# Kernel optimization log

Measured on AMD Instinct MI355X. Metric: run time of the kernel, lower is better.

The kernel has to match this reference:

```python
import jax, jax.numpy as jnp
import numpy as np

V = 50257   # n_unique_words
C = 50257   # n_classes
E = 256     # embed_dim
H = 512     # h_dim
S_IN = 512
S_OUT = 511
START = 1


def setup_inputs() -> dict:
    key = jax.random.key(0)
    ks = jax.random.split(key, 12)
    s = 1.0 / np.sqrt(H)
    u = lambda k, shp: jax.random.uniform(k, shp, jnp.float32, -s, s)
    return {
        "h0": jnp.zeros((1, H), jnp.float32),
        "input_ids": jax.random.randint(ks[0], (1, S_IN), 0, V),
        "output_ids": jax.random.randint(ks[1], (1, S_OUT), 0, V),
        "emb": jax.random.normal(ks[2], (V, E), jnp.float32) * 0.02,
        "enc_wih": u(ks[3], (H, E)),
        "enc_whh": u(ks[4], (H, H)),
        "enc_bih": u(ks[5], (H,)),
        "enc_bhh": u(ks[5], (H,)),
        "dec_wih": u(ks[6], (H, E)),
        "dec_whh": u(ks[7], (H, H)),
        "dec_bih": u(ks[8], (H,)),
        "dec_bhh": u(ks[8], (H,)),
        "fc_w": u(ks[9], (C, H)),
        "fc_b": u(ks[10], (C,)),
    }


def _rnn_cell(x, h, wih, whh, bih, bhh):
    # Elman RNNCell: h' = tanh(x W_ih^T + b_ih + h W_hh^T + b_hh)
    return jnp.tanh(x @ wih.T + bih + h @ whh.T + bhh)


def reference(h0, input_ids, output_ids, emb, enc_wih, enc_whh, enc_bih, enc_bhh,
              dec_wih, dec_whh, dec_bih, dec_bhh, fc_w, fc_b):
    # ---- encode ----
    enc_xs = jnp.swapaxes(emb[input_ids], 0, 1)  # [S_in, 1, E]
    def enc_step(h, x):
        h = _rnn_cell(x, h, enc_wih, enc_whh, enc_bih, enc_bhh)
        return h, None
    hn, _ = jax.lax.scan(enc_step, h0, enc_xs)
    # ---- decode_train ----
    start_emb = emb[jnp.array([START])]          # [1, E]
    h1 = _rnn_cell(start_emb, hn, dec_wih, dec_whh, dec_bih, dec_bhh)
    dec_xs = jnp.swapaxes(emb[output_ids], 0, 1)  # [S_out, 1, E]
    def dec_step(h, x):
        h = _rnn_cell(x, h, dec_wih, dec_whh, dec_bih, dec_bhh)
        return h, h
    _, hs = jax.lax.scan(dec_step, h1, dec_xs)    # [S_out, 1, H]
    pred = jnp.concatenate([h1[None], hs], axis=0)[:, 0, :]  # [S_out+1, H]
    return pred @ fc_w.T + fc_b                   # [S_out+1, C]
```

## Files before the change

kernel.cpp:

```cpp
#include <hip/hip_runtime.h>
#include <hip/hip_fp16.h>

#define EDIM 256
#define HDIM 512
#define CDIM 50257
#define NT_FC 197
#define NJOBS (NT_FC * 4)

using half2_t = __attribute__((ext_vector_type(2))) _Float16;
using half8_t = __attribute__((ext_vector_type(8))) _Float16;
using float4_t = __attribute__((ext_vector_type(4))) float;

__device__ __forceinline__ float dot2(uint32_t w, uint32_t h, float acc) {
    return __builtin_amdgcn_fdot2(__builtin_bit_cast(half2_t, w),
                                  __builtin_bit_cast(half2_t, h), acc, false);
}

__device__ __forceinline__ float fast_tanh(float x) {
    float e = __builtin_amdgcn_exp2f(x * 2.8853900817779268f);
    return 1.f - 2.f * __builtin_amdgcn_rcpf(e + 1.f);
}

__device__ __forceinline__ void scan_body(
    const _Float16* __restrict__ wpack, const float* __restrict__ z,
    const _Float16* __restrict__ h_init, _Float16* __restrict__ hs_out,
    _Float16* __restrict__ hfin_out, int* prog, int nsteps,
    uint4* wlds, uint4* hbuf4) {
    const int tid = threadIdx.x;
    const int c = tid & 15;
    const int g_own = tid >> 3;
    const int hstore = 128 * (g_own & 3) + 8 * (g_own >> 2) + (tid & 7);

    const uint4* wp4 = (const uint4*)wpack;
    uint32_t wreg[192];
#pragma unroll
    for (int g = 0; g < 48; ++g) {
        uint4 v = wp4[g * 512 + tid];
        wreg[g * 4 + 0] = v.x; wreg[g * 4 + 1] = v.y;
        wreg[g * 4 + 2] = v.z; wreg[g * 4 + 3] = v.w;
    }
#pragma unroll
    for (int g = 48; g < 64; ++g) wlds[(g - 48) * 512 + tid] = wp4[g * 512 + tid];

    ((_Float16*)hbuf4)[hstore] = h_init ? h_init[tid] : (_Float16)0.f;
    __syncthreads();

    _Float16 hlast = (_Float16)0.f;
    int cur = 0;
    for (int t = 0; t < nsteps; ++t) {
        float zv = z[t * HDIM + tid];
        const uint4* hb = hbuf4 + cur * 64;
        float acc[16];
#pragma unroll
        for (int r = 0; r < 16; ++r) acc[r] = 0.f;
#pragma unroll
        for (int i = 0; i < 4; ++i) {
            uint4 hg = hb[i * 16 + c];
#pragma unroll
            for (int jr = 0; jr < 12; ++jr) {
                acc[jr] = dot2(wreg[(jr * 4 + i) * 4 + 0], hg.x, acc[jr]);
                acc[jr] = dot2(wreg[(jr * 4 + i) * 4 + 1], hg.y, acc[jr]);
                acc[jr] = dot2(wreg[(jr * 4 + i) * 4 + 2], hg.z, acc[jr]);
                acc[jr] = dot2(wreg[(jr * 4 + i) * 4 + 3], hg.w, acc[jr]);
            }
#pragma unroll
            for (int js = 0; js < 4; ++js) {
                uint4 w = wlds[(js * 4 + i) * 512 + tid];
                acc[12 + js] = dot2(w.x, hg.x, acc[12 + js]);
                acc[12 + js] = dot2(w.y, hg.y, acc[12 + js]);
                acc[12 + js] = dot2(w.z, hg.z, acc[12 + js]);
                acc[12 + js] = dot2(w.w, hg.w, acc[12 + js]);
            }
        }
        float s, keep;
#define FOLD_DPP(aL, aH, bit, ctrl, dst)                                      \
        s = (c & bit) ? (aL) : (aH);                                          \
        s = __builtin_bit_cast(float, __builtin_amdgcn_mov_dpp(               \
                __builtin_bit_cast(int, s), ctrl, 0xF, 0xF, true));           \
        keep = (c & bit) ? (aH) : (aL);                                       \
        dst = keep + s;
#define FOLD_SWZ(aL, aH, bit, pat, dst)                                       \
        s = (c & bit) ? (aL) : (aH);                                          \
        s = __builtin_bit_cast(float, __builtin_amdgcn_ds_swizzle(            \
                __builtin_bit_cast(int, s), pat));                            \
        keep = (c & bit) ? (aH) : (aL);                                       \
        dst = keep + s;
        float b0, b1, b2, b3, b4, b5, b6, b7, d0, d1, d2, d3, e0, e1, v;
        FOLD_DPP(acc[0],  acc[1],  1, 0xB1, b0)
        FOLD_DPP(acc[2],  acc[3],  1, 0xB1, b1)
        FOLD_DPP(acc[4],  acc[5],  1, 0xB1, b2)
        FOLD_DPP(acc[6],  acc[7],  1, 0xB1, b3)
        FOLD_DPP(acc[8],  acc[9],  1, 0xB1, b4)
        FOLD_DPP(acc[10], acc[11], 1, 0xB1, b5)
        FOLD_DPP(acc[12], acc[13], 1, 0xB1, b6)
        FOLD_DPP(acc[14], acc[15], 1, 0xB1, b7)
        FOLD_DPP(b0, b1, 2, 0x4E, d0)
        FOLD_DPP(b2, b3, 2, 0x4E, d1)
        FOLD_DPP(b4, b5, 2, 0x4E, d2)
        FOLD_DPP(b6, b7, 2, 0x4E, d3)
        FOLD_DPP(d0, d2, 8, 0x128, e0)
        FOLD_DPP(d1, d3, 8, 0x128, e1)
        FOLD_SWZ(e0, e1, 4, 0x101F, v)
#undef FOLD_DPP
#undef FOLD_SWZ
        float hnew = fast_tanh(v + zv);
        _Float16 h16v = (_Float16)hnew;
        ((_Float16*)hbuf4)[(cur ^ 1) * 512 + hstore] = h16v;
        if (hs_out) hs_out[t * HDIM + tid] = h16v;
        hlast = h16v;
        __syncthreads();
        if (prog && (t & 127) == 127 && tid == 0) {
            __threadfence();
            __hip_atomic_store(prog, t + 1, __ATOMIC_RELEASE,
                               __HIP_MEMORY_SCOPE_AGENT);
        }
        cur ^= 1;
    }
    if (hfin_out) hfin_out[tid] = hlast;
}

__global__ void __launch_bounds__(256) prep_a(
    const float* __restrict__ enc_whh, _Float16* __restrict__ wpe,
    const int* __restrict__ in_ids, const float* __restrict__ emb,
    const float* __restrict__ enc_wih, const float* __restrict__ enc_bih,
    const float* __restrict__ enc_bhh, float* __restrict__ z,
    int* __restrict__ prog) {
    __shared__ float x[EDIM];
    int b = blockIdx.x;
    if (b == 0 && threadIdx.x == 0)
        __hip_atomic_store(prog, 0, __ATOMIC_RELAXED, __HIP_MEMORY_SCOPE_AGENT);
    if (b < 128) {
        int idx = b * 256 + threadIdx.x;
        int g = idx >> 9, t = idx & 511;
        int jr = g >> 2, i = g & 3;
        int row = ((t >> 4) << 4) + jr;
        int k0 = ((t & 15) << 5) + (i << 3);
        const float* src = enc_whh + row * HDIM + k0;
        uint32_t d[4];
#pragma unroll
        for (int q = 0; q < 4; ++q) {
            half2_t p;
            p[0] = (_Float16)src[2 * q];
            p[1] = (_Float16)src[2 * q + 1];
            d[q] = __builtin_bit_cast(uint32_t, p);
        }
        ((uint4*)wpe)[g * 512 + t] = make_uint4(d[0], d[1], d[2], d[3]);
    } else {
        int t = b - 128;
        int id = in_ids[t];
        x[threadIdx.x] = emb[(long)id * EDIM + threadIdx.x];
        __syncthreads();
#pragma unroll
        for (int rr = 0; rr < 2; ++rr) {
            int r = threadIdx.x + rr * 256;
            const float4* w4 = (const float4*)(enc_wih + r * EDIM);
            float acc = 0.f;
#pragma unroll 8
            for (int k4 = 0; k4 < 64; ++k4) {
                float4 wv = w4[k4];
                acc += wv.x * x[k4 * 4 + 0] + wv.y * x[k4 * 4 + 1] +
                       wv.z * x[k4 * 4 + 2] + wv.w * x[k4 * 4 + 3];
            }
            z[t * HDIM + r] = acc + enc_bih[r] + enc_bhh[r];
        }
    }
}

__global__ void __launch_bounds__(512, 2) enc_fused(
    const _Float16* __restrict__ wpe, const float* __restrict__ z,
    _Float16* __restrict__ hn16,
    const float* __restrict__ dec_whh, _Float16* __restrict__ wpd,
    const int* __restrict__ out_ids, const float* __restrict__ emb,
    const float* __restrict__ dec_wih, const float* __restrict__ dec_bih,
    const float* __restrict__ dec_bhh, float* __restrict__ zf,
    const float* __restrict__ fc_w, _Float16* __restrict__ fcw16, long fcw_n) {
    __shared__ uint4 wlds[16 * 512];
    __shared__ uint4 hbuf4[2 * 64];
    int b = blockIdx.x, tid = threadIdx.x;
    if (b == 0) {
        scan_body(wpe, z, nullptr, nullptr, hn16, nullptr, 512, wlds, hbuf4);
    } else if (b < 65) {
        int idx = (b - 1) * 512 + tid;
        int g = idx >> 9, t = idx & 511;
        int jr = g >> 2, i = g & 3;
        int row = ((t >> 4) << 4) + jr;
        int k0 = ((t & 15) << 5) + (i << 3);
        const float* src = dec_whh + row * HDIM + k0;
        uint32_t d[4];
#pragma unroll
        for (int q = 0; q < 4; ++q) {
            half2_t p;
            p[0] = (_Float16)src[2 * q];
            p[1] = (_Float16)src[2 * q + 1];
            d[q] = __builtin_bit_cast(uint32_t, p);
        }
        ((uint4*)wpd)[g * 512 + t] = make_uint4(d[0], d[1], d[2], d[3]);
    } else if (b < 577) {
        int t = 512 + (b - 65);
        float* x = (float*)wlds;
        int id = (t == 512) ? 1 : out_ids[t - 513];
        if (tid < EDIM) x[tid] = emb[(long)id * EDIM + tid];
        __syncthreads();
        const float4* w4 = (const float4*)(dec_wih + tid * EDIM);
        float acc = 0.f;
#pragma unroll 8
        for (int k4 = 0; k4 < 64; ++k4) {
            float4 wv = w4[k4];
            acc += wv.x * x[k4 * 4 + 0] + wv.y * x[k4 * 4 + 1] +
                   wv.z * x[k4 * 4 + 2] + wv.w * x[k4 * 4 + 3];
        }
        zf[t * HDIM + tid] = acc + dec_bih[tid] + dec_bhh[tid];
    } else {
        long i = ((long)(b - 577) * 512 + tid) * 8;
        if (i + 8 <= fcw_n) {
            const float4* s4 = (const float4*)(fc_w + i);
            float4 a = s4[0], bb = s4[1];
            half8_t o;
            o[0] = (_Float16)a.x;  o[1] = (_Float16)a.y;
            o[2] = (_Float16)a.z;  o[3] = (_Float16)a.w;
            o[4] = (_Float16)bb.x; o[5] = (_Float16)bb.y;
            o[6] = (_Float16)bb.z; o[7] = (_Float16)bb.w;
            *(half8_t*)(fcw16 + i) = o;
        }
    }
}

__global__ void __launch_bounds__(512, 2) dec_fc(
    const _Float16* __restrict__ wpd, const float* __restrict__ zdec,
    const _Float16* __restrict__ hn16, _Float16* __restrict__ h16,
    int* __restrict__ prog,
    const _Float16* __restrict__ Bw16, const float* __restrict__ Bw32,
    int use16, const float* __restrict__ bias, float* __restrict__ out) {
    __shared__ uint4 wlds[16 * 512];
    __shared__ uint4 hbuf4[2 * 64];
    int b = blockIdx.x, tid = threadIdx.x;
    if (b == 0) {
        scan_body(wpd, zdec, hn16, h16, nullptr, prog, 512, wlds, hbuf4);
        return;
    }
    int w = tid >> 6, l = tid & 63;
    int wm = (w >> 2) * 64, wn = (w & 3) * 64;
    int lr = l & 15, lk = (l >> 4) * 8;
    for (int j = b - 1; j < NJOBS; j += 255) {
        int mj = j / NT_FC, nj = j - mj * NT_FC;
        if (tid == 0) {
            int need = (mj + 1) * 128;
            while (__hip_atomic_load(prog, __ATOMIC_RELAXED,
                                     __HIP_MEMORY_SCOPE_AGENT) < need)
                __builtin_amdgcn_s_sleep(64);
            __threadfence();
        }
        __syncthreads();
        int m0 = mj * 128, n0 = nj * 256;
        float4_t acc[4][4];
#pragma unroll
        for (int fm = 0; fm < 4; ++fm)
#pragma unroll
            for (int fn = 0; fn < 4; ++fn)
                acc[fm][fn] = (float4_t){0.f, 0.f, 0.f, 0.f};
        for (int ks = 0; ks < 512; ks += 32) {
            half8_t a[4], bf[4];
#pragma unroll
            for (int f = 0; f < 4; ++f) {
                int m = m0 + wm + f * 16 + lr;
                a[f] = *(const half8_t*)(h16 + (long)m * 512 + ks + lk);
                int n = n0 + wn + f * 16 + lr;
                if (n < CDIM) {
                    if (use16) {
                        bf[f] = *(const half8_t*)(Bw16 + (long)n * 512 + ks + lk);
                    } else {
                        const float4* bp4 =
                            (const float4*)(Bw32 + (long)n * 512 + ks + lk);
                        float4 x0 = bp4[0], x1 = bp4[1];
                        half8_t bb;
                        bb[0] = (_Float16)x0.x; bb[1] = (_Float16)x0.y;
                        bb[2] = (_Float16)x0.z; bb[3] = (_Float16)x0.w;
                        bb[4] = (_Float16)x1.x; bb[5] = (_Float16)x1.y;
                        bb[6] = (_Float16)x1.z; bb[7] = (_Float16)x1.w;
                        bf[f] = bb;
                    }
                } else {
#pragma unroll
                    for (int e = 0; e < 8; ++e) bf[f][e] = (_Float16)0.f;
                }
            }
#pragma unroll
            for (int fm = 0; fm < 4; ++fm)
#pragma unroll
                for (int fn = 0; fn < 4; ++fn)
                    acc[fm][fn] = __builtin_amdgcn_mfma_f32_16x16x32_f16(
                        a[fm], bf[fn], acc[fm][fn], 0, 0, 0);
        }
#pragma unroll
        for (int fn = 0; fn < 4; ++fn) {
            int n = n0 + wn + fn * 16 + lr;
            if (n >= CDIM) continue;
            float bv = bias[n];
#pragma unroll
            for (int fm = 0; fm < 4; ++fm) {
#pragma unroll
                for (int q = 0; q < 4; ++q) {
                    int m = m0 + wm + fm * 16 + (l >> 4) * 4 + q;
                    out[(long)m * CDIM + n] = acc[fm][fn][q] + bv;
                }
            }
        }
    }
}

extern "C" void kernel_launch(void* const* d_in, const int* in_sizes, int n_in,
                              void* d_out, int out_size, void* d_ws, size_t ws_size,
                              hipStream_t stream) {
    const int* input_ids  = (const int*)d_in[1];
    const int* output_ids = (const int*)d_in[2];
    const float* emb      = (const float*)d_in[3];
    const float* enc_wih  = (const float*)d_in[4];
    const float* enc_whh  = (const float*)d_in[5];
    const float* enc_bih  = (const float*)d_in[6];
    const float* enc_bhh  = (const float*)d_in[7];
    const float* dec_wih  = (const float*)d_in[8];
    const float* dec_whh  = (const float*)d_in[9];
    const float* dec_bih  = (const float*)d_in[10];
    const float* dec_bhh  = (const float*)d_in[11];
    const float* fc_w     = (const float*)d_in[12];
    const float* fc_b     = (const float*)d_in[13];
    float* out = (float*)d_out;

    char* ws = (char*)d_ws;
    float* z        = (float*)ws;
    _Float16* wpe   = (_Float16*)(ws + (2u << 20));
    _Float16* wpd   = (_Float16*)(ws + (2u << 20) + (512u << 10));
    _Float16* h16   = (_Float16*)(ws + (3u << 20));
    _Float16* hn16  = (_Float16*)(ws + (3u << 20) + (512u << 10));
    int* prog       = (int*)(ws + (3u << 20) + (513u << 10));
    _Float16* fcw16 = (_Float16*)(ws + (4u << 20));

    const long fcw_n = (long)CDIM * HDIM;
    bool use_f16_fc = ws_size >= (size_t)(4u << 20) + (size_t)fcw_n * 2;
    int nb_cvt = use_f16_fc ? (int)((fcw_n / 8 + 511) / 512) : 0;

    prep_a<<<640, 256, 0, stream>>>(enc_whh, wpe, input_ids, emb,
                                    enc_wih, enc_bih, enc_bhh, z, prog);
    enc_fused<<<577 + nb_cvt, 512, 0, stream>>>(
        wpe, z, hn16, dec_whh, wpd, output_ids, emb,
        dec_wih, dec_bih, dec_bhh, z, fc_w, fcw16, fcw_n);
    dec_fc<<<256, 512, 0, stream>>>(wpd, z + 512 * HDIM, hn16, h16, prog,
                                    fcw16, fc_w, use_f16_fc ? 1 : 0,
                                    fc_b, out);
}
```

Before: 1.492 ms.

## Split each RNN scan across two workgroups with global flag handshakes

Both the encoder and decoder recurrences now run on two workgroups, each owning half of the hidden rows and keeping its half of W_hh fully in registers. The hidden state is exchanged through global memory double buffers, and per-step release/acquire flags synchronise the pair. This halves the per-step dot-product work and removes the LDS-resident weight slice, but adds a cross-CU spin-wait and global round trip on every one of the 1024 sequential steps. The FC consumers now wait on both decoder flags, and block indices are remapped, presumably so the two scan blocks land on different XCDs or CUs.

```diff
diff --git a/kernel.cpp b/kernel.cpp
--- a/kernel.cpp
+++ b/kernel.cpp
@@ -21,57 +21,48 @@
     return 1.f - 2.f * __builtin_amdgcn_rcpf(e + 1.f);
 }
 
-__device__ __forceinline__ void scan_body(
-    const _Float16* __restrict__ wpack, const float* __restrict__ z,
-    const _Float16* __restrict__ h_init, _Float16* __restrict__ hs_out,
-    _Float16* __restrict__ hfin_out, int* prog, int nsteps,
-    uint4* wlds, uint4* hbuf4) {
+__device__ __forceinline__ void scan2_body(
+    const uint4* __restrict__ wp4,
+    const float* __restrict__ z,
+    _Float16* __restrict__ hxA, _Float16* __restrict__ hxB,
+    int* myflag, int* pflag,
+    _Float16* __restrict__ hs_out,
+    _Float16* __restrict__ hfin_out,
+    int hb2, int nsteps) {
     const int tid = threadIdx.x;
-    const int c = tid & 15;
-    const int g_own = tid >> 3;
-    const int hstore = 128 * (g_own & 3) + 8 * (g_own >> 2) + (tid & 7);
-
-    const uint4* wp4 = (const uint4*)wpack;
-    uint32_t wreg[192];
-#pragma unroll
-    for (int g = 0; g < 48; ++g) {
-        uint4 v = wp4[g * 512 + tid];
-        wreg[g * 4 + 0] = v.x; wreg[g * 4 + 1] = v.y;
-        wreg[g * 4 + 2] = v.z; wreg[g * 4 + 3] = v.w;
-    }
-#pragma unroll
-    for (int g = 48; g < 64; ++g) wlds[(g - 48) * 512 + tid] = wp4[g * 512 + tid];
-
-    ((_Float16*)hbuf4)[hstore] = h_init ? h_init[tid] : (_Float16)0.f;
-    __syncthreads();
-
-    _Float16 hlast = (_Float16)0.f;
-    int cur = 0;
+    const int c = tid & 15, rg = tid >> 4;
+    const int grow = hb2 * 256 + rg * 8 + (c & 7);
+
+    uint4 wreg4[32];
+#pragma unroll
+    for (int g = 0; g < 32; ++g) wreg4[g] = wp4[g * 512 + tid];
+
     for (int t = 0; t < nsteps; ++t) {
-        float zv = z[t * HDIM + tid];
-        const uint4* hb = hbuf4 + cur * 64;
-        float acc[16];
-#pragma unroll
-        for (int r = 0; r < 16; ++r) acc[r] = 0.f;
-#pragma unroll
-        for (int i = 0; i < 4; ++i) {
-            uint4 hg = hb[i * 16 + c];
-#pragma unroll
-            for (int jr = 0; jr < 12; ++jr) {
-                acc[jr] = dot2(wreg[(jr * 4 + i) * 4 + 0], hg.x, acc[jr]);
-                acc[jr] = dot2(wreg[(jr * 4 + i) * 4 + 1], hg.y, acc[jr]);
-                acc[jr] = dot2(wreg[(jr * 4 + i) * 4 + 2], hg.z, acc[jr]);
-                acc[jr] = dot2(wreg[(jr * 4 + i) * 4 + 3], hg.w, acc[jr]);
-            }
-#pragma unroll
-            for (int js = 0; js < 4; ++js) {
-                uint4 w = wlds[(js * 4 + i) * 512 + tid];
-                acc[12 + js] = dot2(w.x, hg.x, acc[12 + js]);
-                acc[12 + js] = dot2(w.y, hg.y, acc[12 + js]);
-                acc[12 + js] = dot2(w.z, hg.z, acc[12 + js]);
-                acc[12 + js] = dot2(w.w, hg.w, acc[12 + js]);
-            }
-        }
+        if (tid == 0) {
+            while (__hip_atomic_load(pflag, __ATOMIC_RELAXED,
+                                     __HIP_MEMORY_SCOPE_AGENT) < t) {}
+            __threadfence();
+        }
+        __syncthreads();
+        const _Float16* hcur = (t & 1) ? hxB : hxA;
+        _Float16*       hnxt = (t & 1) ? hxA : hxB;
+        float zv = z[t * HDIM + grow];
+        uint4 hg0 = ((const uint4*)hcur)[c * 4 + 0];
+        uint4 hg1 = ((const uint4*)hcur)[c * 4 + 1];
+        uint4 hg2 = ((const uint4*)hcur)[c * 4 + 2];
+        uint4 hg3 = ((const uint4*)hcur)[c * 4 + 3];
+
+        float acc[8] = {0.f, 0.f, 0.f, 0.f, 0.f, 0.f, 0.f, 0.f};
+#define MAC_I(I, HG)                                                          \
+        _Pragma("unroll")                                                     \
+        for (int jr = 0; jr < 8; ++jr) {                                      \
+            acc[jr] = dot2(wreg4[jr * 4 + I].x, HG.x, acc[jr]);               \
+            acc[jr] = dot2(wreg4[jr * 4 + I].y, HG.y, acc[jr]);               \
+            acc[jr] = dot2(wreg4[jr * 4 + I].z, HG.z, acc[jr]);               \
+            acc[jr] = dot2(wreg4[jr * 4 + I].w, HG.w, acc[jr]);               \
+        }
+        MAC_I(0, hg0) MAC_I(1, hg1) MAC_I(2, hg2) MAC_I(3, hg3)
+#undef MAC_I
         float s, keep;
 #define FOLD_DPP(aL, aH, bit, ctrl, dst)                                      \
         s = (c & bit) ? (aL) : (aH);                                          \
@@ -79,125 +70,113 @@
                 __builtin_bit_cast(int, s), ctrl, 0xF, 0xF, true));           \
         keep = (c & bit) ? (aH) : (aL);                                       \
         dst = keep + s;
-#define FOLD_SWZ(aL, aH, bit, pat, dst)                                       \
-        s = (c & bit) ? (aL) : (aH);                                          \
-        s = __builtin_bit_cast(float, __builtin_amdgcn_ds_swizzle(            \
-                __builtin_bit_cast(int, s), pat));                            \
-        keep = (c & bit) ? (aH) : (aL);                                       \
-        dst = keep + s;
-        float b0, b1, b2, b3, b4, b5, b6, b7, d0, d1, d2, d3, e0, e1, v;
-        FOLD_DPP(acc[0],  acc[1],  1, 0xB1, b0)
-        FOLD_DPP(acc[2],  acc[3],  1, 0xB1, b1)
-        FOLD_DPP(acc[4],  acc[5],  1, 0xB1, b2)
-        FOLD_DPP(acc[6],  acc[7],  1, 0xB1, b3)
-        FOLD_DPP(acc[8],  acc[9],  1, 0xB1, b4)
-        FOLD_DPP(acc[10], acc[11], 1, 0xB1, b5)
-        FOLD_DPP(acc[12], acc[13], 1, 0xB1, b6)
-        FOLD_DPP(acc[14], acc[15], 1, 0xB1, b7)
-        FOLD_DPP(b0, b1, 2, 0x4E, d0)
-        FOLD_DPP(b2, b3, 2, 0x4E, d1)
-        FOLD_DPP(b4, b5, 2, 0x4E, d2)
-        FOLD_DPP(b6, b7, 2, 0x4E, d3)
-        FOLD_DPP(d0, d2, 8, 0x128, e0)
-        FOLD_DPP(d1, d3, 8, 0x128, e1)
-        FOLD_SWZ(e0, e1, 4, 0x101F, v)
+        float f0, f1, f2, f3, g0, g1, e, v;
+        FOLD_DPP(acc[0], acc[1], 1, 0xB1, f0)
+        FOLD_DPP(acc[2], acc[3], 1, 0xB1, f1)
+        FOLD_DPP(acc[4], acc[5], 1, 0xB1, f2)
+        FOLD_DPP(acc[6], acc[7], 1, 0xB1, f3)
+        FOLD_DPP(f0, f1, 2, 0x4E, g0)
+        FOLD_DPP(f2, f3, 2, 0x4E, g1)
+        s = (c & 4) ? g0 : g1;
+        s = __builtin_bit_cast(float, __builtin_amdgcn_ds_swizzle(
+                __builtin_bit_cast(int, s), 0x101F));
+        keep = (c & 4) ? g1 : g0;
+        e = keep + s;
+        s = __builtin_bit_cast(float, __builtin_amdgcn_mov_dpp(
+                __builtin_bit_cast(int, e), 0x128, 0xF, 0xF, true));
+        v = e + s;
 #undef FOLD_DPP
-#undef FOLD_SWZ
         float hnew = fast_tanh(v + zv);
         _Float16 h16v = (_Float16)hnew;
-        ((_Float16*)hbuf4)[(cur ^ 1) * 512 + hstore] = h16v;
-        if (hs_out) hs_out[t * HDIM + tid] = h16v;
-        hlast = h16v;
+        if (c < 8) {
+            hnxt[grow] = h16v;
+            if (hs_out) hs_out[t * HDIM + grow] = h16v;
+            if (hfin_out && t == nsteps - 1) hfin_out[grow] = h16v;
+        }
         __syncthreads();
-        if (prog && (t & 127) == 127 && tid == 0) {
-            __threadfence();
-            __hip_atomic_store(prog, t + 1, __ATOMIC_RELEASE,
+        if (tid == 0)
+            __hip_atomic_store(myflag, t + 1, __ATOMIC_RELEASE,
                                __HIP_MEMORY_SCOPE_AGENT);
-        }
-        cur ^= 1;
-    }
-    if (hfin_out) hfin_out[tid] = hlast;
-}
-
-__global__ void __launch_bounds__(256) prep_a(
+    }
+}
+
+__device__ __forceinline__ void pack_one(const float* __restrict__ whh,
+                                         _Float16* __restrict__ wp, int G) {
+    int hb2 = G >> 14, g = (G >> 9) & 31, tt = G & 511;
+    int row = hb2 * 256 + ((tt >> 4) << 3) + (g >> 2);
+    int k0 = ((tt & 15) << 5) + ((g & 3) << 3);
+    const float* src = whh + row * HDIM + k0;
+    uint32_t d[4];
+#pragma unroll
+    for (int q = 0; q < 4; ++q) {
+        half2_t p;
+        p[0] = (_Float16)src[2 * q];
+        p[1] = (_Float16)src[2 * q + 1];
+        d[q] = __builtin_bit_cast(uint32_t, p);
+    }
+    ((uint4*)wp)[G] = make_uint4(d[0], d[1], d[2], d[3]);
+}
+
+__global__ void __launch_bounds__(512) prep_a(
     const float* __restrict__ enc_whh, _Float16* __restrict__ wpe,
     const int* __restrict__ in_ids, const float* __restrict__ emb,
     const float* __restrict__ enc_wih, const float* __restrict__ enc_bih,
     const float* __restrict__ enc_bhh, float* __restrict__ z,
-    int* __restrict__ prog) {
+    int* __restrict__ flags, _Float16* __restrict__ hx_enc) {
     __shared__ float x[EDIM];
-    int b = blockIdx.x;
-    if (b == 0 && threadIdx.x == 0)
-        __hip_atomic_store(prog, 0, __ATOMIC_RELAXED, __HIP_MEMORY_SCOPE_AGENT);
-    if (b < 128) {
-        int idx = b * 256 + threadIdx.x;
-        int g = idx >> 9, t = idx & 511;
-        int jr = g >> 2, i = g & 3;
-        int row = ((t >> 4) << 4) + jr;
-        int k0 = ((t & 15) << 5) + (i << 3);
-        const float* src = enc_whh + row * HDIM + k0;
-        uint32_t d[4];
-#pragma unroll
-        for (int q = 0; q < 4; ++q) {
-            half2_t p;
-            p[0] = (_Float16)src[2 * q];
-            p[1] = (_Float16)src[2 * q + 1];
-            d[q] = __builtin_bit_cast(uint32_t, p);
-        }
-        ((uint4*)wpe)[g * 512 + t] = make_uint4(d[0], d[1], d[2], d[3]);
-    } else {
-        int t = b - 128;
-        int id = in_ids[t];
-        x[threadIdx.x] = emb[(long)id * EDIM + threadIdx.x];
-        __syncthreads();
-#pragma unroll
-        for (int rr = 0; rr < 2; ++rr) {
-            int r = threadIdx.x + rr * 256;
-            const float4* w4 = (const float4*)(enc_wih + r * EDIM);
-            float acc = 0.f;
+    int b = blockIdx.x, tid = threadIdx.x;
+    if (b == 0) {
+        if (tid < 128)
+            __hip_atomic_store(flags + tid, 0, __ATOMIC_RELAXED,
+                               __HIP_MEMORY_SCOPE_AGENT);
+        hx_enc[tid] = (_Float16)0.f;
+        return;
+    }
+    if (b < 65) {
+        pack_one(enc_whh, wpe, (b - 1) * 512 + tid);
+        return;
+    }
+    int t = b - 65;
+    int id = in_ids[t];
+    if (tid < EDIM) x[tid] = emb[(long)id * EDIM + tid];
+    __syncthreads();
+    const float4* w4 = (const float4*)(enc_wih + tid * EDIM);
+    float acc = 0.f;
 #pragma unroll 8
-            for (int k4 = 0; k4 < 64; ++k4) {
-                float4 wv = w4[k4];
-                acc += wv.x * x[k4 * 4 + 0] + wv.y * x[k4 * 4 + 1] +
-                       wv.z * x[k4 * 4 + 2] + wv.w * x[k4 * 4 + 3];
-            }
-            z[t * HDIM + r] = acc + enc_bih[r] + enc_bhh[r];
-        }
-    }
+    for (int k4 = 0; k4 < 64; ++k4) {
+        float4 wv = w4[k4];
+        acc += wv.x * x[k4 * 4 + 0] + wv.y * x[k4 * 4 + 1] +
+               wv.z * x[k4 * 4 + 2] + wv.w * x[k4 * 4 + 3];
+    }
+    z[t * HDIM + tid] = acc + enc_bih[tid] + enc_bhh[tid];
 }
 
 __global__ void __launch_bounds__(512, 2) enc_fused(
     const _Float16* __restrict__ wpe, const float* __restrict__ z,
-    _Float16* __restrict__ hn16,
+    int* __restrict__ flags,
+    _Float16* __restrict__ hx_enc, _Float16* __restrict__ hx_dec,
     const float* __restrict__ dec_whh, _Float16* __restrict__ wpd,
     const int* __restrict__ out_ids, const float* __restrict__ emb,
     const float* __restrict__ dec_wih, const float* __restrict__ dec_bih,
     const float* __restrict__ dec_bhh, float* __restrict__ zf,
     const float* __restrict__ fc_w, _Float16* __restrict__ fcw16, long fcw_n) {
-    __shared__ uint4 wlds[16 * 512];
-    __shared__ uint4 hbuf4[2 * 64];
+    __shared__ uint4 ldsbig[16 * 512];
     int b = blockIdx.x, tid = threadIdx.x;
-    if (b == 0) {
-        scan_body(wpe, z, nullptr, nullptr, hn16, nullptr, 512, wlds, hbuf4);
-    } else if (b < 65) {
-        int idx = (b - 1) * 512 + tid;
-        int g = idx >> 9, t = idx & 511;
-        int jr = g >> 2, i = g & 3;
-        int row = ((t >> 4) << 4) + jr;
-        int k0 = ((t & 15) << 5) + (i << 3);
-        const float* src = dec_whh + row * HDIM + k0;
-        uint32_t d[4];
-#pragma unroll
-        for (int q = 0; q < 4; ++q) {
-            half2_t p;
-            p[0] = (_Float16)src[2 * q];
-            p[1] = (_Float16)src[2 * q + 1];
-            d[q] = __builtin_bit_cast(uint32_t, p);
-        }
-        ((uint4*)wpd)[g * 512 + t] = make_uint4(d[0], d[1], d[2], d[3]);
-    } else if (b < 577) {
-        int t = 512 + (b - 65);
-        float* x = (float*)wlds;
+    if (tid == 511) *(volatile unsigned int*)&ldsbig[0] = 0u;
+    if (b == 0 || b == 8) {
+        int hb2 = (b == 8) ? 1 : 0;
+        scan2_body((const uint4*)wpe + hb2 * 32 * 512, z,
+                   hx_enc, hx_enc + 512,
+                   flags + hb2 * 32, flags + (1 - hb2) * 32,
+                   nullptr, hx_dec, hb2, 512);
+        return;
+    }
+    int jb = (b < 8) ? b - 1 : b - 2;
+    if (jb < 64) {
+        pack_one(dec_whh, wpd, jb * 512 + tid);
+    } else if (jb < 576) {
+        int t = 512 + (jb - 64);
+        float* x = (float*)ldsbig;
         int id = (t == 512) ? 1 : out_ids[t - 513];
         if (tid < EDIM) x[tid] = emb[(long)id * EDIM + tid];
         __syncthreads();
@@ -211,7 +190,7 @@
         }
         zf[t * HDIM + tid] = acc + dec_bih[tid] + dec_bhh[tid];
     } else {
-        long i = ((long)(b - 577) * 512 + tid) * 8;
+        long i = ((long)(jb - 576) * 512 + tid) * 8;
         if (i + 8 <= fcw_n) {
             const float4* s4 = (const float4*)(fc_w + i);
             float4 a = s4[0], bb = s4[1];
@@ -227,25 +206,35 @@
 
 __global__ void __launch_bounds__(512, 2) dec_fc(
     const _Float16* __restrict__ wpd, const float* __restrict__ zdec,
-    const _Float16* __restrict__ hn16, _Float16* __restrict__ h16,
-    int* __restrict__ prog,
+    _Float16* __restrict__ hx_dec, _Float16* __restrict__ h16,
+    int* __restrict__ flags,
     const _Float16* __restrict__ Bw16, const float* __restrict__ Bw32,
     int use16, const float* __restrict__ bias, float* __restrict__ out) {
-    __shared__ uint4 wlds[16 * 512];
-    __shared__ uint4 hbuf4[2 * 64];
+    __shared__ uint4 ldsbig[16 * 512];
     int b = blockIdx.x, tid = threadIdx.x;
-    if (b == 0) {
-        scan_body(wpd, zdec, hn16, h16, nullptr, prog, 512, wlds, hbuf4);
+    if (tid == 511) *(volatile unsigned int*)&ldsbig[0] = 0u;
+    int* decf0 = flags + 64;
+    int* decf1 = flags + 96;
+    if (b == 0 || b == 8) {
+        int hb2 = (b == 8) ? 1 : 0;
+        scan2_body((const uint4*)wpd + hb2 * 32 * 512, zdec,
+                   hx_dec, hx_dec + 512,
+                   (hb2 ? decf1 : decf0), (hb2 ? decf0 : decf1),
+                   h16, nullptr, hb2, 512);
         return;
     }
+    if ((b & 7) == 0) return;
+    int di = b - (b >> 3) - 1;
     int w = tid >> 6, l = tid & 63;
     int wm = (w >> 2) * 64, wn = (w & 3) * 64;
     int lr = l & 15, lk = (l >> 4) * 8;
-    for (int j = b - 1; j < NJOBS; j += 255) {
+    for (int j = di; j < NJOBS; j += 224) {
         int mj = j / NT_FC, nj = j - mj * NT_FC;
         if (tid == 0) {
             int need = (mj + 1) * 128;
-            while (__hip_atomic_load(prog, __ATOMIC_RELAXED,
+            while (__hip_atomic_load(decf0, __ATOMIC_RELAXED,
+                                     __HIP_MEMORY_SCOPE_AGENT) < need ||
+                   __hip_atomic_load(decf1, __ATOMIC_RELAXED,
                                      __HIP_MEMORY_SCOPE_AGENT) < need)
                 __builtin_amdgcn_s_sleep(64);
             __threadfence();
@@ -331,20 +320,23 @@
     _Float16* wpe   = (_Float16*)(ws + (2u << 20));
     _Float16* wpd   = (_Float16*)(ws + (2u << 20) + (512u << 10));
     _Float16* h16   = (_Float16*)(ws + (3u << 20));
-    _Float16* hn16  = (_Float16*)(ws + (3u << 20) + (512u << 10));
-    int* prog       = (int*)(ws + (3u << 20) + (513u << 10));
+    int* flags      = (int*)(ws + (3u << 20) + (512u << 10));
+    _Float16* hx_enc = (_Float16*)(ws + (3u << 20) + (512u << 10) + 512);
+    _Float16* hx_dec = (_Float16*)(ws + (3u << 20) + (512u << 10) + 2560);
     _Float16* fcw16 = (_Float16*)(ws + (4u << 20));
 
     const long fcw_n = (long)CDIM * HDIM;
     bool use_f16_fc = ws_size >= (size_t)(4u << 20) + (size_t)fcw_n * 2;
     int nb_cvt = use_f16_fc ? (int)((fcw_n / 8 + 511) / 512) : 0;
 
-    prep_a<<<640, 256, 0, stream>>>(enc_whh, wpe, input_ids, emb,
-                                    enc_wih, enc_bih, enc_bhh, z, prog);
-    enc_fused<<<577 + nb_cvt, 512, 0, stream>>>(
-        wpe, z, hn16, dec_whh, wpd, output_ids, emb,
+    prep_a<<<577, 512, 0, stream>>>(enc_whh, wpe, input_ids, emb,
+                                    enc_wih, enc_bih, enc_bhh, z,
+                                    flags, hx_enc);
+    enc_fused<<<578 + nb_cvt, 512, 0, stream>>>(
+        wpe, z, flags, hx_enc, hx_dec,
+        dec_whh, wpd, output_ids, emb,
         dec_wih, dec_bih, dec_bhh, z, fc_w, fcw16, fcw_n);
-    dec_fc<<<256, 512, 0, stream>>>(wpd, z + 512 * HDIM, hn16, h16, prog,
+    dec_fc<<<256, 512, 0, stream>>>(wpd, z + 512 * HDIM, hx_dec, h16, flags,
                                     fcw16, fc_w, use_f16_fc ? 1 : 0,
                                     fc_b, out);
 }
```

Measured after the change: 2.124 ms (median of 2 runs). +42.4%, slower.

## Swizzle packed RNN weights to simplify reduction and idle every eighth FC block

Applied to the files above, without the earlier changes.

The recurrent weight packing now XORs the row index with the lane-in-group, so each lane's partial sums already line up for a simple DPP add tree. This drops the select/keep pairs around every reduction step on the serial scan's critical path. The FC consumer blocks also change: every eighth block exits immediately (after a dummy LDS write), leaving 224 worker blocks. The likely aim is to free the XCD or CU that hosts the scan block from contention, at the cost of less FC throughput.

```diff
diff --git a/kernel.cpp b/kernel.cpp
--- a/kernel.cpp
+++ b/kernel.cpp
@@ -19,6 +19,23 @@
 __device__ __forceinline__ float fast_tanh(float x) {
     float e = __builtin_amdgcn_exp2f(x * 2.8853900817779268f);
     return 1.f - 2.f * __builtin_amdgcn_rcpf(e + 1.f);
+}
+
+__device__ __forceinline__ void pack_one(const float* __restrict__ whh,
+                                         _Float16* __restrict__ wp,
+                                         int g, int t) {
+    int row = ((t >> 4) << 4) + ((g >> 2) ^ (t & 15));
+    int k0 = ((t & 15) << 5) + ((g & 3) << 3);
+    const float* src = whh + row * HDIM + k0;
+    uint32_t d[4];
+#pragma unroll
+    for (int q = 0; q < 4; ++q) {
+        half2_t p;
+        p[0] = (_Float16)src[2 * q];
+        p[1] = (_Float16)src[2 * q + 1];
+        d[q] = __builtin_bit_cast(uint32_t, p);
+    }
+    ((uint4*)wp)[g * 512 + t] = make_uint4(d[0], d[1], d[2], d[3]);
 }
 
 __device__ __forceinline__ void scan_body(
@@ -50,60 +67,55 @@
     for (int t = 0; t < nsteps; ++t) {
         float zv = z[t * HDIM + tid];
         const uint4* hb = hbuf4 + cur * 64;
-        float acc[16];
-#pragma unroll
-        for (int r = 0; r < 16; ++r) acc[r] = 0.f;
+        float f[16];
+#pragma unroll
+        for (int r = 0; r < 16; ++r) f[r] = 0.f;
 #pragma unroll
         for (int i = 0; i < 4; ++i) {
             uint4 hg = hb[i * 16 + c];
 #pragma unroll
-            for (int jr = 0; jr < 12; ++jr) {
-                acc[jr] = dot2(wreg[(jr * 4 + i) * 4 + 0], hg.x, acc[jr]);
-                acc[jr] = dot2(wreg[(jr * 4 + i) * 4 + 1], hg.y, acc[jr]);
-                acc[jr] = dot2(wreg[(jr * 4 + i) * 4 + 2], hg.z, acc[jr]);
-                acc[jr] = dot2(wreg[(jr * 4 + i) * 4 + 3], hg.w, acc[jr]);
+            for (int s = 0; s < 12; ++s) {
+                f[s] = dot2(wreg[(s * 4 + i) * 4 + 0], hg.x, f[s]);
+                f[s] = dot2(wreg[(s * 4 + i) * 4 + 1], hg.y, f[s]);
+                f[s] = dot2(wreg[(s * 4 + i) * 4 + 2], hg.z, f[s]);
+                f[s] = dot2(wreg[(s * 4 + i) * 4 + 3], hg.w, f[s]);
             }
 #pragma unroll
             for (int js = 0; js < 4; ++js) {
                 uint4 w = wlds[(js * 4 + i) * 512 + tid];
-                acc[12 + js] = dot2(w.x, hg.x, acc[12 + js]);
-                acc[12 + js] = dot2(w.y, hg.y, acc[12 + js]);
-                acc[12 + js] = dot2(w.z, hg.z, acc[12 + js]);
-                acc[12 + js] = dot2(w.w, hg.w, acc[12 + js]);
-            }
-        }
-        float s, keep;
-#define FOLD_DPP(aL, aH, bit, ctrl, dst)                                      \
-        s = (c & bit) ? (aL) : (aH);                                          \
-        s = __builtin_bit_cast(float, __builtin_amdgcn_mov_dpp(               \
-                __builtin_bit_cast(int, s), ctrl, 0xF, 0xF, true));           \
-        keep = (c & bit) ? (aH) : (aL);                                       \
-        dst = keep + s;
-#define FOLD_SWZ(aL, aH, bit, pat, dst)                                       \
-        s = (c & bit) ? (aL) : (aH);                                          \
-        s = __builtin_bit_cast(float, __builtin_amdgcn_ds_swizzle(            \
-                __builtin_bit_cast(int, s), pat));                            \
-        keep = (c & bit) ? (aH) : (aL);                                       \
-        dst = keep + s;
-        float b0, b1, b2, b3, b4, b5, b6, b7, d0, d1, d2, d3, e0, e1, v;
-        FOLD_DPP(acc[0],  acc[1],  1, 0xB1, b0)
-        FOLD_DPP(acc[2],  acc[3],  1, 0xB1, b1)
-        FOLD_DPP(acc[4],  acc[5],  1, 0xB1, b2)
-        FOLD_DPP(acc[6],  acc[7],  1, 0xB1, b3)
-        FOLD_DPP(acc[8],  acc[9],  1, 0xB1, b4)
-        FOLD_DPP(acc[10], acc[11], 1, 0xB1, b5)
-        FOLD_DPP(acc[12], acc[13], 1, 0xB1, b6)
-        FOLD_DPP(acc[14], acc[15], 1, 0xB1, b7)
-        FOLD_DPP(b0, b1, 2, 0x4E, d0)
-        FOLD_DPP(b2, b3, 2, 0x4E, d1)
-        FOLD_DPP(b4, b5, 2, 0x4E, d2)
-        FOLD_DPP(b6, b7, 2, 0x4E, d3)
-        FOLD_DPP(d0, d2, 8, 0x128, e0)
-        FOLD_DPP(d1, d3, 8, 0x128, e1)
-        FOLD_SWZ(e0, e1, 4, 0x101F, v)
-#undef FOLD_DPP
-#undef FOLD_SWZ
-        float hnew = fast_tanh(v + zv);
+                f[12 + js] = dot2(w.x, hg.x, f[12 + js]);
+                f[12 + js] = dot2(w.y, hg.y, f[12 + js]);
+                f[12 + js] = dot2(w.z, hg.z, f[12 + js]);
+                f[12 + js] = dot2(w.w, hg.w, f[12 + js]);
+            }
+        }
+#define DPPADD(DST, A, B, CTRL) {                                             \
+        int _x = __builtin_amdgcn_mov_dpp(__builtin_bit_cast(int, (B)),       \
+                                          CTRL, 0xF, 0xF, true);              \
+        DST = (A) + __builtin_bit_cast(float, _x); }
+        float t0, t2, t4, t6, t8, t10, t12, t14;
+        DPPADD(t0,  f[0],  f[1],  0xB1)
+        DPPADD(t2,  f[2],  f[3],  0xB1)
+        DPPADD(t4,  f[4],  f[5],  0xB1)
+        DPPADD(t6,  f[6],  f[7],  0xB1)
+        DPPADD(t8,  f[8],  f[9],  0xB1)
+        DPPADD(t10, f[10], f[11], 0xB1)
+        DPPADD(t12, f[12], f[13], 0xB1)
+        DPPADD(t14, f[14], f[15], 0xB1)
+        float u0, u4, u8, u12;
+        DPPADD(u0,  t0,  t2,  0x4E)
+        DPPADD(u4,  t4,  t6,  0x4E)
+        DPPADD(u8,  t8,  t10, 0x4E)
+        DPPADD(u12, t12, t14, 0x4E)
+        float v0, v4;
+        DPPADD(v0, u0, u8,  0x128)
+        DPPADD(v4, u4, u12, 0x128)
+#undef DPPADD
+        float sw = __builtin_bit_cast(float, __builtin_amdgcn_ds_swizzle(
+                       __builtin_bit_cast(int, v4), 0x101F));
+        float vfin = v0 + sw;
+
+        float hnew = fast_tanh(vfin + zv);
         _Float16 h16v = (_Float16)hnew;
         ((_Float16*)hbuf4)[(cur ^ 1) * 512 + hstore] = h16v;
         if (hs_out) hs_out[t * HDIM + tid] = h16v;
@@ -131,20 +143,7 @@
         __hip_atomic_store(prog, 0, __ATOMIC_RELAXED, __HIP_MEMORY_SCOPE_AGENT);
     if (b < 128) {
         int idx = b * 256 + threadIdx.x;
-        int g = idx >> 9, t = idx & 511;
-        int jr = g >> 2, i = g & 3;
-        int row = ((t >> 4) << 4) + jr;
-        int k0 = ((t & 15) << 5) + (i << 3);
-        const float* src = enc_whh + row * HDIM + k0;
-        uint32_t d[4];
-#pragma unroll
-        for (int q = 0; q < 4; ++q) {
-            half2_t p;
-            p[0] = (_Float16)src[2 * q];
-            p[1] = (_Float16)src[2 * q + 1];
-            d[q] = __builtin_bit_cast(uint32_t, p);
-        }
-        ((uint4*)wpe)[g * 512 + t] = make_uint4(d[0], d[1], d[2], d[3]);
+        pack_one(enc_whh, wpe, idx >> 9, idx & 511);
     } else {
         int t = b - 128;
         int id = in_ids[t];
@@ -181,20 +180,7 @@
         scan_body(wpe, z, nullptr, nullptr, hn16, nullptr, 512, wlds, hbuf4);
     } else if (b < 65) {
         int idx = (b - 1) * 512 + tid;
-        int g = idx >> 9, t = idx & 511;
-        int jr = g >> 2, i = g & 3;
-        int row = ((t >> 4) << 4) + jr;
-        int k0 = ((t & 15) << 5) + (i << 3);
-        const float* src = dec_whh + row * HDIM + k0;
-        uint32_t d[4];
-#pragma unroll
-        for (int q = 0; q < 4; ++q) {
-            half2_t p;
-            p[0] = (_Float16)src[2 * q];
-            p[1] = (_Float16)src[2 * q + 1];
-            d[q] = __builtin_bit_cast(uint32_t, p);
-        }
-        ((uint4*)wpd)[g * 512 + t] = make_uint4(d[0], d[1], d[2], d[3]);
+        pack_one(dec_whh, wpd, idx >> 9, idx & 511);
     } else if (b < 577) {
         int t = 512 + (b - 65);
         float* x = (float*)wlds;
@@ -238,10 +224,13 @@
         scan_body(wpd, zdec, hn16, h16, nullptr, prog, 512, wlds, hbuf4);
         return;
     }
+    if (tid == 511) *(volatile unsigned int*)&wlds[0] = 0u;
+    if ((b & 7) == 0) return;
+    int di = b - (b >> 3) - 1;
     int w = tid >> 6, l = tid & 63;
     int wm = (w >> 2) * 64, wn = (w & 3) * 64;
     int lr = l & 15, lk = (l >> 4) * 8;
-    for (int j = b - 1; j < NJOBS; j += 255) {
+    for (int j = di; j < NJOBS; j += 224) {
         int mj = j / NT_FC, nj = j - mj * NT_FC;
         if (tid == 0) {
             int need = (mj + 1) * 128;
```

New measurement: 1.366 ms. 8.4% less time.
